# Kernel optimization log

Hardware: AMD Instinct MI355X
Metric: run time of the kernel (lower is better)

Reference implementation:

```python
import jax, jax.numpy as jnp
import numpy as np
import math

B, H, L, DK, D, LOCAL = 4, 8, 2048, 64, 512, 4


def setup_inputs() -> dict:
    key = jax.random.key(0)
    ks = jax.random.split(key, 9)
    n = L
    return {
        'query': jax.random.normal(ks[0], (B, H, L, DK), jnp.float32),
        'key': jax.random.normal(ks[1], (B, H, L, DK), jnp.float32),
        'value': jax.random.normal(ks[2], (B, H, L, DK), jnp.float32),
        'users': jax.random.normal(ks[3], (B, L, D), jnp.float32),
        'mask': jnp.tril(jnp.ones((L, L), dtype=bool))[None, None],  # causal [1,1,L,L]
        'rel_pos_w': jax.random.normal(ks[4], (2 * n - 1, DK * LOCAL), jnp.float32) * 0.02,
        'user_proj_w': jax.random.normal(ks[5], (DK * LOCAL, D), jnp.float32) * 0.02,
        'user_proj_b': jax.random.normal(ks[6], (DK * LOCAL,), jnp.float32) * 0.02,
        'mlp_w': jax.random.normal(ks[7], (LOCAL, DK), jnp.float32) * 0.1,
        'mlp_b': jax.random.normal(ks[8], (LOCAL,), jnp.float32) * 0.1,
    }


def reference(query, key, value, users, mask, rel_pos_w, user_proj_w, user_proj_b, mlp_w, mlp_b):
    b, h, l, dk = query.shape
    local = mlp_w.shape[0]
    g = h - local
    n = l
    scale = 1.0 / math.sqrt(dk)
    NEG = -1e12  # MAX_VAL in the torch source

    # ---- global heads: plain softmax attention ----
    qg, kg, vg = query[:, :g], key[:, :g], value[:, :g]
    sg = jnp.einsum('bhqd,bhkd->bhqk', qg, kg) * scale
    sg = jnp.where(mask, sg, NEG)
    pg = jax.nn.softmax(sg, axis=-1)
    og = jnp.einsum('bhqk,bhkd->bhqd', pg, vg)

    # ---- local (LOCKER) heads ----
    ql, kl, vl = query[:, g:], key[:, g:], value[:, g:]
    sl = jnp.einsum('bhqd,bhkd->bhqk', ql, kl) * scale

    # reweight = Linear(d_k,1)(rel_pos + v_q + v_k + user_proj(users)_q) per local head.
    # Linear over a sum decomposes exactly (same math, avoids [b,local,l,l,dk] tensor):
    rel_tab = rel_pos_w.reshape(2 * n - 1, local, dk)
    rel_scores = jnp.einsum('rhd,hd->rh', rel_tab, mlp_w)          # [2n-1, local]
    pos = jnp.arange(n)
    distance = pos[None, :] - pos[:, None] + n - 1                  # [l, l]
    rel_term = rel_scores[distance].transpose(2, 0, 1)              # [local, l, l]

    v_term = jnp.einsum('bhkd,hd->bhk', vl, mlp_w)                  # [b, local, l]
    u = (users @ user_proj_w.T + user_proj_b).reshape(b, l, local, dk)
    u_term = jnp.einsum('bqhd,hd->bhq', u, mlp_w)                   # [b, local, l]

    reweight = (rel_term[None]
                + v_term[:, :, None, :]      # value_l.unsqueeze(-3): varies over key idx
                + v_term[:, :, :, None]      # value_l.unsqueeze(-2): varies over query idx
                + u_term[:, :, :, None]      # user term broadcast over key idx
                + mlp_b[None, :, None, None])

    sl = sl + reweight
    sl = jnp.where(mask, sl, NEG)
    pl = jax.nn.softmax(sl, axis=-1)
    ol = jnp.einsum('bhqk,bhkd->bhqd', pl, vl)

    return jnp.concatenate([og, ol], axis=1)  # [b, h, l, d_k]
```

## Files before the change

### kernel.cpp

```cpp
#include <hip/hip_runtime.h>

#define TL 2048
#define NHEAD 8
#define NLOC 4
#define L2E 1.44269504f
#define PSTRIDE 4352

typedef __attribute__((ext_vector_type(4))) float f32x4;
typedef __attribute__((ext_vector_type(16))) float f32x16;
typedef __attribute__((ext_vector_type(8))) __bf16 bf16x8;
typedef __attribute__((ext_vector_type(8))) unsigned short u16x8;
typedef __attribute__((ext_vector_type(4))) unsigned int u32x4;

static __device__ __forceinline__ unsigned short f2bf(float f) {
    unsigned u = __float_as_uint(f);
    u = (u + 0x7FFFu + ((u >> 16) & 1u)) >> 16;
    return (unsigned short)u;
}
static __device__ __forceinline__ unsigned int cvtpk(float a, float b) {
    unsigned int w;
    asm("v_cvt_pk_bf16_f32 %0, %1, %2" : "=v"(w) : "v"(a), "v"(b));
    return w;
}

__global__ __launch_bounds__(256) void preconv_kernel(
    const float* __restrict__ key, const float* __restrict__ value,
    const float* __restrict__ mlp_w, const float* __restrict__ rel_pos_w,
    unsigned short* __restrict__ Kb, unsigned short* __restrict__ Vtb,
    float* __restrict__ vtbf, float* __restrict__ rel_sf) {
    int blk = blockIdx.x;
    int t = threadIdx.x;
    int wave = t >> 6, lane = t & 63;

    if (blk >= 1024) {
        int r = (blk - 1024) * 4 + wave;
        if (r < 2 * TL - 1) {
#pragma unroll
            for (int hp = 0; hp < 4; ++hp) {
                float v = rel_pos_w[r * 256 + hp * 64 + lane] * mlp_w[hp * 64 + lane];
#pragma unroll
                for (int off = 32; off; off >>= 1) v += __shfl_xor(v, off);
                if (lane == 0) rel_sf[hp * 4096 + r] = v * L2E;
            }
        }
        return;
    }

    __shared__ float Tf[64][66];
    int bh = blk >> 5, kt = blk & 31;
    int h = bh & 7, b = bh >> 3;
    size_t src = (size_t)blk * 4096;
    size_t dst = (size_t)blk * 4096;

    {
        int row = t >> 2, q4 = t & 3;
        const float* kp = key + src + row * 64 + q4 * 16;
#pragma unroll
        for (int j = 0; j < 4; ++j)
            *(f32x4*)&Tf[row][q4 * 16 + j * 4] = *(const f32x4*)(kp + j * 4);
    }
    __syncthreads();
#pragma unroll
    for (int i = 0; i < 2; ++i) {
        int idx = t + i * 256;
        int l31 = idx & 31, hi = (idx >> 5) & 1, mq = (idx >> 6) & 3, h2 = idx >> 8;
        int r = h2 * 32 + l31, c = mq * 2 + hi;
        u16x8 o;
#pragma unroll
        for (int j = 0; j < 8; ++j) o[j] = f2bf(Tf[r][c * 8 + j]);
        *(u16x8*)&Kb[dst + idx * 8] = o;
    }
    __syncthreads();

    {
        int row = t >> 2, q4 = t & 3;
        const float* vp = value + src + row * 64 + q4 * 16;
#pragma unroll
        for (int j = 0; j < 4; ++j)
            *(f32x4*)&Tf[row][q4 * 16 + j * 4] = *(const f32x4*)(vp + j * 4);
    }
    __syncthreads();
#pragma unroll
    for (int i = 0; i < 2; ++i) {
        int idx = t + i * 256;
        int l31 = idx & 31, hi = (idx >> 5) & 1, half = (idx >> 6) & 1, c2 = idx >> 7;
        int r = half * 32 + l31, c = c2 * 2 + hi;
        u16x8 o;
#pragma unroll
        for (int j = 0; j < 8; ++j) o[j] = f2bf(Tf[c * 8 + j][r]);
        *(u16x8*)&Vtb[dst + idx * 8] = o;
    }
    if (h >= NLOC) {
        float mw = mlp_w[(h - NLOC) * 64 + lane];
        float* vout = vtbf + (size_t)((b * NLOC + h - NLOC) * TL) + kt * 64;
#pragma unroll
        for (int i = 0; i < 16; ++i) {
            int row = wave * 16 + i;
            float v = Tf[row][lane] * mw;
#pragma unroll
            for (int off = 32; off; off >>= 1) v += __shfl_xor(v, off);
            if (lane == 0) vout[row] = v * L2E;
        }
    }
}

#define MFMA32(A, B, C) __builtin_amdgcn_mfma_f32_32x32x16_bf16(A, B, C, 0, 0, 0)

__global__ __launch_bounds__(256, 4) void attn_kernel(
    const float* __restrict__ query,
    const unsigned short* __restrict__ Kb, const unsigned short* __restrict__ Vtb,
    const float* __restrict__ rel_sf, const float* __restrict__ vtbf,
    float* __restrict__ part) {

    __shared__ float relw[384];

    int bid = blockIdx.x;
    int bhx = bid & 31;
    int bh = (bhx & 7) * 4 + (bhx >> 3);
    int sid = bid >> 5;
    int i = 0, s = 0, acc = 0;
    for (int ii = 15; ii >= 0; --ii) {
        int ns = (2 * ii + 4) / 3;
        if (sid >= acc && sid < acc + ns) { i = ii; s = sid - acc; }
        acc += ns;
    }
    int nt = 2 * i + 2;
    int n = (2 * i + 4) / 3;
    int T = nt / n, R = nt % n;
    int k_b = s * T + min(s, R);
    int len = T + (s < R ? 1 : 0);
    int q0 = i << 7;

    int h = bh & 7, b = bh >> 3;
    bool islocal = (h >= NLOC);
    int t = threadIdx.x;
    int w = t >> 6;
    int l31 = t & 31;
    int hi = (t >> 5) & 1;
    int qrel = 32 * w + l31;
    int qglob = q0 + qrel;
    int qmaxw = q0 + 32 * w + 31;
    int hivl = hi * 256 + l31 * 8;

    size_t tbase = (size_t)bh * 32 * 4096;
    const unsigned short* Ktiles = Kb + tbase;
    const unsigned short* Vtiles = Vtb + tbase;
    const float* vtpf = vtbf + (islocal ? (size_t)((b * NLOC + h - NLOC) * TL) : 0);
    int idxlo = 64 * k_b - q0 + 1920;
    const float* relsrc = rel_sf + (islocal ? ((h - NLOC) * 4096 + idxlo) : 0);

    if (islocal && t < 96) ((f32x4*)relw)[t] = ((const f32x4*)relsrc)[t];

    const float SC = 0.125f * L2E;
    bf16x8 qf[4];
    {
        const float* qsrc = query + ((size_t)bh * TL + qglob) * 64 + 8 * hi;
#pragma unroll
        for (int mq = 0; mq < 4; ++mq) {
            f32x4 a = *(const f32x4*)(qsrc + 16 * mq);
            f32x4 c = *(const f32x4*)(qsrc + 16 * mq + 4);
            u16x8 u;
#pragma unroll
            for (int j = 0; j < 4; ++j) { u[j] = f2bf(a[j] * SC); u[4 + j] = f2bf(c[j] * SC); }
            qf[mq] = __builtin_bit_cast(bf16x8, u);
        }
    }

    float m = -1e30f, lsum = 0.f;
    f32x16 O0 = {0,0,0,0,0,0,0,0,0,0,0,0,0,0,0,0};
    f32x16 O1 = {0,0,0,0,0,0,0,0,0,0,0,0,0,0,0,0};

    __syncthreads();

#pragma unroll 1
    for (int kt4 = 0; kt4 < len; ++kt4) {
        int kt = k_b + kt4;
        if (64 * kt > qmaxw) break;
        const unsigned short* Kt = Ktiles + (size_t)kt * 4096;
        const unsigned short* Vt = Vtiles + (size_t)kt * 4096;
        const float* bias = vtpf + kt * 64;
        bool maskt = (64 * kt + 63 > q0 + 32 * w);

#pragma unroll
        for (int h2 = 0; h2 < 2; ++h2) {
            f32x16 S;
            if (islocal) {
                int rbase = 64 * kt4 + 32 * h2 + 4 * hi + 127 - qrel;
#pragma unroll
                for (int g = 0; g < 4; ++g) {
                    f32x4 bv = *(const f32x4*)&bias[32 * h2 + 8 * g + 4 * hi];
#pragma unroll
                    for (int j = 0; j < 4; ++j)
                        S[4 * g + j] = bv[j] + relw[rbase + 8 * g + j];
                }
            } else {
                S = (f32x16){0,0,0,0,0,0,0,0,0,0,0,0,0,0,0,0};
            }
            __builtin_amdgcn_s_setprio(1);
#pragma unroll
            for (int mq = 0; mq < 4; ++mq) {
                const bf16x8 kf = *(const bf16x8*)&Kt[(h2 * 4 + mq) * 512 + hivl];
                S = MFMA32(kf, qf[mq], S);
            }
            __builtin_amdgcn_s_setprio(0);

            if (maskt) {
                int koff = 64 * kt + 32 * h2 + 4 * hi - qglob;
#pragma unroll
                for (int r = 0; r < 16; ++r) {
                    int kk = (r & 3) + 8 * (r >> 2);
                    if (koff + kk > 0) S[r] = -1e30f;
                }
            }
            float pmax = -1e30f;
#pragma unroll
            for (int r = 0; r < 16; ++r) pmax = fmaxf(pmax, S[r]);
            pmax = fmaxf(pmax, __shfl_xor(pmax, 32));
            if (__any(pmax > m + 11.5f)) {
                float nm2 = fmaxf(m, pmax);
                float corr = exp2f(m - nm2);
                lsum *= corr;
#pragma unroll
                for (int r = 0; r < 16; ++r) { O0[r] *= corr; O1[r] *= corr; }
                m = nm2;
            }
            float ps = 0.f;
#pragma unroll
            for (int r = 0; r < 16; ++r) {
                float p = exp2f(S[r] - m);
                S[r] = p; ps += p;
            }
            ps += __shfl_xor(ps, 32);
            lsum += ps;

            __builtin_amdgcn_s_setprio(1);
#pragma unroll
            for (int kq = 0; kq < 2; ++kq) {
                int ra = 8 * kq;
                unsigned int x0 = cvtpk(S[ra + 0], S[ra + 1]);
                unsigned int x1 = cvtpk(S[ra + 2], S[ra + 3]);
                unsigned int y0 = cvtpk(S[ra + 4], S[ra + 5]);
                unsigned int y1 = cvtpk(S[ra + 6], S[ra + 7]);
                asm("v_permlane32_swap_b32 %0, %1" : "+v"(x0), "+v"(y0));
                asm("v_permlane32_swap_b32 %0, %1" : "+v"(x1), "+v"(y1));
                u32x4 fw;
                fw[0] = x0; fw[1] = x1; fw[2] = y0; fw[3] = y1;
                const bf16x8 pf = __builtin_bit_cast(bf16x8, fw);
                int c2 = h2 * 2 + kq;
                const bf16x8 vf0 = *(const bf16x8*)&Vt[c2 * 1024 + hivl];
                const bf16x8 vf1 = *(const bf16x8*)&Vt[c2 * 1024 + 512 + hivl];
                O0 = MFMA32(vf0, pf, O0);
                O1 = MFMA32(vf1, pf, O1);
            }
            __builtin_amdgcn_s_setprio(0);
        }
    }

    float* pp = part + (size_t)bid * PSTRIDE;
    unsigned int* po = (unsigned int*)pp;
#pragma unroll
    for (int g = 0; g < 4; ++g) {
        unsigned int w0 = cvtpk(O0[4 * g + 0], O0[4 * g + 1]);
        unsigned int w1 = cvtpk(O0[4 * g + 2], O0[4 * g + 3]);
        unsigned int w2 = cvtpk(O1[4 * g + 0], O1[4 * g + 1]);
        unsigned int w3 = cvtpk(O1[4 * g + 2], O1[4 * g + 3]);
        int dp0 = 4 * g + 2 * hi;
        po[dp0 * 128 + qrel] = w0;
        po[(dp0 + 1) * 128 + qrel] = w1;
        po[(16 + dp0) * 128 + qrel] = w2;
        po[(16 + dp0 + 1) * 128 + qrel] = w3;
    }
    if (hi == 0) { pp[4096 + qrel] = m; pp[4224 + qrel] = lsum; }
}

__global__ __launch_bounds__(128) void merge_kernel(
    const float* __restrict__ part, float* __restrict__ out) {
    int bid = blockIdx.x;
    int bhx = bid & 31, i = bid >> 5;
    int bh = (bhx & 7) * 4 + (bhx >> 3);
    int n = (2 * i + 4) / 3;
    int sb = 0;
    for (int ii = 15; ii > i; --ii) sb += (2 * ii + 4) / 3;
    int t = threadIdx.x;

    float mv[11], lv[11];
#pragma unroll
    for (int s2 = 0; s2 < 11; ++s2) {
        mv[s2] = -1e30f; lv[s2] = 0.f;
        if (s2 < n) {
            const float* pp = part + (size_t)((sb + s2) * 32 + bhx) * PSTRIDE;
            mv[s2] = pp[4096 + t]; lv[s2] = pp[4224 + t];
        }
    }
    float nm = mv[0];
#pragma unroll
    for (int s2 = 1; s2 < 11; ++s2) nm = fmaxf(nm, mv[s2]);
    float den = 0.f;
    float cw[11];
#pragma unroll
    for (int s2 = 0; s2 < 11; ++s2) { cw[s2] = exp2f(mv[s2] - nm); den += lv[s2] * cw[s2]; }
    float inv = 1.0f / den;
#pragma unroll
    for (int s2 = 0; s2 < 11; ++s2) cw[s2] *= inv;

    size_t obase = (size_t)bh * TL * 64 + (size_t)(128 * i + t) * 64;
    for (int seg = 0; seg < 4; ++seg) {
        float o[16];
#pragma unroll
        for (int j = 0; j < 16; ++j) o[j] = 0.f;
#pragma unroll
        for (int s2 = 0; s2 < 11; ++s2) {
            if (s2 < n) {
                const unsigned int* po =
                    (const unsigned int*)(part + (size_t)((sb + s2) * 32 + bhx) * PSTRIDE);
                float wsc = cw[s2];
#pragma unroll
                for (int j = 0; j < 8; ++j) {
                    unsigned int wv = po[(seg * 8 + j) * 128 + t];
                    o[2 * j]     += wsc * __uint_as_float((wv & 0xffffu) << 16);
                    o[2 * j + 1] += wsc * __uint_as_float(wv & 0xffff0000u);
                }
            }
        }
#pragma unroll
        for (int c = 0; c < 4; ++c)
            *(f32x4*)(out + obase + seg * 16 + 4 * c) = *(const f32x4*)&o[4 * c];
    }
}

extern "C" void kernel_launch(void* const* d_in, const int* in_sizes, int n_in,
                              void* d_out, int out_size, void* d_ws, size_t ws_size,
                              hipStream_t stream) {
    const float* query = (const float*)d_in[0];
    const float* key = (const float*)d_in[1];
    const float* value = (const float*)d_in[2];
    const float* rel_pos_w = (const float*)d_in[5];
    const float* mlp_w = (const float*)d_in[8];
    float* out = (float*)d_out;

    unsigned short* Kb = (unsigned short*)d_ws;
    unsigned short* Vtb = Kb + 32 * 32 * 4096;
    float* rel_sf = (float*)(Vtb + 32 * 32 * 4096);
    float* vtbf = rel_sf + 4 * 4096;
    float* part = vtbf + 32768;

    preconv_kernel<<<2048, 256, 0, stream>>>(key, value, mlp_w, rel_pos_w,
                                             Kb, Vtb, vtbf, rel_sf);
    attn_kernel<<<3072, 256, 0, stream>>>(query, Kb, Vtb, rel_sf, vtbf, part);
    merge_kernel<<<512, 128, 0, stream>>>(part, out);
}
```

Measured before the change: 90.48 us.

## Double-buffer K/V tiles in LDS via async global loads and halve KV splits

Attention blocks now stage each K and V tile into LDS with global_load_lds in a double buffer, prefetching the next tile while the current one is computed, and synchronising once per tile. The number of KV splits per query block roughly halves, giving a smaller grid where each block handles more tiles and the merge kernel combines fewer partials. This targets global-load latency and split/merge overhead, at the cost of about 34KB of LDS per block (lower occupancy), a barrier per tile, and less parallelism.

```diff
diff --git a/kernel.cpp b/kernel.cpp
--- a/kernel.cpp
+++ b/kernel.cpp
@@ -21,6 +21,11 @@
     unsigned int w;
     asm("v_cvt_pk_bf16_f32 %0, %1, %2" : "=v"(w) : "v"(a), "v"(b));
     return w;
+}
+static __device__ __forceinline__ void gl_lds16(const void* g, void* l) {
+    __builtin_amdgcn_global_load_lds(
+        (const __attribute__((address_space(1))) void*)g,
+        (__attribute__((address_space(3))) void*)l, 16, 0, 0);
 }
 
 __global__ __launch_bounds__(256) void preconv_kernel(
@@ -112,7 +117,10 @@
     const float* __restrict__ rel_sf, const float* __restrict__ vtbf,
     float* __restrict__ part) {
 
-    __shared__ float relw[384];
+    __shared__ __align__(16) unsigned char smem[34816];
+    unsigned short* Ks0 = (unsigned short*)smem;
+    unsigned short* Vt0 = (unsigned short*)(smem + 16384);
+    float* relw = (float*)(smem + 32768);
 
     int bid = blockIdx.x;
     int bhx = bid & 31;
@@ -120,12 +128,12 @@
     int sid = bid >> 5;
     int i = 0, s = 0, acc = 0;
     for (int ii = 15; ii >= 0; --ii) {
-        int ns = (2 * ii + 4) / 3;
+        int ns = (2 * ii + 7) / 6;
         if (sid >= acc && sid < acc + ns) { i = ii; s = sid - acc; }
         acc += ns;
     }
     int nt = 2 * i + 2;
-    int n = (2 * i + 4) / 3;
+    int n = (2 * i + 7) / 6;
     int T = nt / n, R = nt % n;
     int k_b = s * T + min(s, R);
     int len = T + (s < R ? 1 : 0);
@@ -149,7 +157,11 @@
     int idxlo = 64 * k_b - q0 + 1920;
     const float* relsrc = rel_sf + (islocal ? ((h - NLOC) * 4096 + idxlo) : 0);
 
-    if (islocal && t < 96) ((f32x4*)relw)[t] = ((const f32x4*)relsrc)[t];
+    gl_lds16(Ktiles + (size_t)k_b * 4096 + t * 8, Ks0 + t * 8);
+    gl_lds16(Ktiles + (size_t)k_b * 4096 + 2048 + t * 8, Ks0 + 2048 + t * 8);
+    gl_lds16(Vtiles + (size_t)k_b * 4096 + t * 8, Vt0 + t * 8);
+    gl_lds16(Vtiles + (size_t)k_b * 4096 + 2048 + t * 8, Vt0 + 2048 + t * 8);
+    if (islocal && t < 128) ((f32x4*)relw)[t] = ((const f32x4*)relsrc)[t];
 
     const float SC = 0.125f * L2E;
     bf16x8 qf[4];
@@ -172,88 +184,103 @@
 
     __syncthreads();
 
+    int cur = 0;
 #pragma unroll 1
     for (int kt4 = 0; kt4 < len; ++kt4) {
         int kt = k_b + kt4;
-        if (64 * kt > qmaxw) break;
-        const unsigned short* Kt = Ktiles + (size_t)kt * 4096;
-        const unsigned short* Vt = Vtiles + (size_t)kt * 4096;
+        unsigned short* Ks = Ks0 + cur * 4096;
+        unsigned short* Vt = Vt0 + cur * 4096;
         const float* bias = vtpf + kt * 64;
+
+        if (kt4 + 1 < len) {
+            int nb = cur ^ 1;
+            const unsigned short* gk = Ktiles + (size_t)(kt + 1) * 4096;
+            const unsigned short* gv = Vtiles + (size_t)(kt + 1) * 4096;
+            gl_lds16(gk + t * 8, Ks0 + nb * 4096 + t * 8);
+            gl_lds16(gk + 2048 + t * 8, Ks0 + nb * 4096 + 2048 + t * 8);
+            gl_lds16(gv + t * 8, Vt0 + nb * 4096 + t * 8);
+            gl_lds16(gv + 2048 + t * 8, Vt0 + nb * 4096 + 2048 + t * 8);
+        }
+
+        bool active = (64 * kt <= qmaxw);
         bool maskt = (64 * kt + 63 > q0 + 32 * w);
-
-#pragma unroll
-        for (int h2 = 0; h2 < 2; ++h2) {
-            f32x16 S;
-            if (islocal) {
-                int rbase = 64 * kt4 + 32 * h2 + 4 * hi + 127 - qrel;
-#pragma unroll
-                for (int g = 0; g < 4; ++g) {
-                    f32x4 bv = *(const f32x4*)&bias[32 * h2 + 8 * g + 4 * hi];
-#pragma unroll
-                    for (int j = 0; j < 4; ++j)
-                        S[4 * g + j] = bv[j] + relw[rbase + 8 * g + j];
-                }
-            } else {
-                S = (f32x16){0,0,0,0,0,0,0,0,0,0,0,0,0,0,0,0};
+        if (active) {
+#pragma unroll
+            for (int h2 = 0; h2 < 2; ++h2) {
+                f32x16 S;
+                if (islocal) {
+                    int rbase = 64 * kt4 + 32 * h2 + 4 * hi + 127 - qrel;
+#pragma unroll
+                    for (int g = 0; g < 4; ++g) {
+                        f32x4 bv = *(const f32x4*)&bias[32 * h2 + 8 * g + 4 * hi];
+#pragma unroll
+                        for (int j = 0; j < 4; ++j)
+                            S[4 * g + j] = bv[j] + relw[rbase + 8 * g + j];
+                    }
+                } else {
+                    S = (f32x16){0,0,0,0,0,0,0,0,0,0,0,0,0,0,0,0};
+                }
+                __builtin_amdgcn_s_setprio(1);
+#pragma unroll
+                for (int mq = 0; mq < 4; ++mq) {
+                    const bf16x8 kf = *(const bf16x8*)&Ks[(h2 * 4 + mq) * 512 + hivl];
+                    S = MFMA32(kf, qf[mq], S);
+                }
+                __builtin_amdgcn_s_setprio(0);
+
+                if (maskt) {
+                    int koff = 64 * kt + 32 * h2 + 4 * hi - qglob;
+#pragma unroll
+                    for (int r = 0; r < 16; ++r) {
+                        int kk = (r & 3) + 8 * (r >> 2);
+                        if (koff + kk > 0) S[r] = -1e30f;
+                    }
+                }
+                float pmax = -1e30f;
+#pragma unroll
+                for (int r = 0; r < 16; ++r) pmax = fmaxf(pmax, S[r]);
+                pmax = fmaxf(pmax, __shfl_xor(pmax, 32));
+                if (__any(pmax > m + 11.5f)) {
+                    float nm2 = fmaxf(m, pmax);
+                    float corr = exp2f(m - nm2);
+                    lsum *= corr;
+#pragma unroll
+                    for (int r = 0; r < 16; ++r) { O0[r] *= corr; O1[r] *= corr; }
+                    m = nm2;
+                }
+                float ps = 0.f;
+#pragma unroll
+                for (int r = 0; r < 16; ++r) {
+                    float p = exp2f(S[r] - m);
+                    S[r] = p; ps += p;
+                }
+                ps += __shfl_xor(ps, 32);
+                lsum += ps;
+
+                __builtin_amdgcn_s_setprio(1);
+#pragma unroll
+                for (int kq = 0; kq < 2; ++kq) {
+                    int ra = 8 * kq;
+                    unsigned int x0 = cvtpk(S[ra + 0], S[ra + 1]);
+                    unsigned int x1 = cvtpk(S[ra + 2], S[ra + 3]);
+                    unsigned int y0 = cvtpk(S[ra + 4], S[ra + 5]);
+                    unsigned int y1 = cvtpk(S[ra + 6], S[ra + 7]);
+                    asm("v_permlane32_swap_b32 %0, %1" : "+v"(x0), "+v"(y0));
+                    asm("v_permlane32_swap_b32 %0, %1" : "+v"(x1), "+v"(y1));
+                    u32x4 fw;
+                    fw[0] = x0; fw[1] = x1; fw[2] = y0; fw[3] = y1;
+                    const bf16x8 pf = __builtin_bit_cast(bf16x8, fw);
+                    int c2 = h2 * 2 + kq;
+                    const bf16x8 vf0 = *(const bf16x8*)&Vt[c2 * 1024 + hivl];
+                    const bf16x8 vf1 = *(const bf16x8*)&Vt[c2 * 1024 + 512 + hivl];
+                    O0 = MFMA32(vf0, pf, O0);
+                    O1 = MFMA32(vf1, pf, O1);
+                }
+                __builtin_amdgcn_s_setprio(0);
             }
-            __builtin_amdgcn_s_setprio(1);
-#pragma unroll
-            for (int mq = 0; mq < 4; ++mq) {
-                const bf16x8 kf = *(const bf16x8*)&Kt[(h2 * 4 + mq) * 512 + hivl];
-                S = MFMA32(kf, qf[mq], S);
-            }
-            __builtin_amdgcn_s_setprio(0);
-
-            if (maskt) {
-                int koff = 64 * kt + 32 * h2 + 4 * hi - qglob;
-#pragma unroll
-                for (int r = 0; r < 16; ++r) {
-                    int kk = (r & 3) + 8 * (r >> 2);
-                    if (koff + kk > 0) S[r] = -1e30f;
-                }
-            }
-            float pmax = -1e30f;
-#pragma unroll
-            for (int r = 0; r < 16; ++r) pmax = fmaxf(pmax, S[r]);
-            pmax = fmaxf(pmax, __shfl_xor(pmax, 32));
-            if (__any(pmax > m + 11.5f)) {
-                float nm2 = fmaxf(m, pmax);
-                float corr = exp2f(m - nm2);
-                lsum *= corr;
-#pragma unroll
-                for (int r = 0; r < 16; ++r) { O0[r] *= corr; O1[r] *= corr; }
-                m = nm2;
-            }
-            float ps = 0.f;
-#pragma unroll
-            for (int r = 0; r < 16; ++r) {
-                float p = exp2f(S[r] - m);
-                S[r] = p; ps += p;
-            }
-            ps += __shfl_xor(ps, 32);
-            lsum += ps;
-
-            __builtin_amdgcn_s_setprio(1);
-#pragma unroll
-            for (int kq = 0; kq < 2; ++kq) {
-                int ra = 8 * kq;
-                unsigned int x0 = cvtpk(S[ra + 0], S[ra + 1]);
-                unsigned int x1 = cvtpk(S[ra + 2], S[ra + 3]);
-                unsigned int y0 = cvtpk(S[ra + 4], S[ra + 5]);
-                unsigned int y1 = cvtpk(S[ra + 6], S[ra + 7]);
-                asm("v_permlane32_swap_b32 %0, %1" : "+v"(x0), "+v"(y0));
-                asm("v_permlane32_swap_b32 %0, %1" : "+v"(x1), "+v"(y1));
-                u32x4 fw;
-                fw[0] = x0; fw[1] = x1; fw[2] = y0; fw[3] = y1;
-                const bf16x8 pf = __builtin_bit_cast(bf16x8, fw);
-                int c2 = h2 * 2 + kq;
-                const bf16x8 vf0 = *(const bf16x8*)&Vt[c2 * 1024 + hivl];
-                const bf16x8 vf1 = *(const bf16x8*)&Vt[c2 * 1024 + 512 + hivl];
-                O0 = MFMA32(vf0, pf, O0);
-                O1 = MFMA32(vf1, pf, O1);
-            }
-            __builtin_amdgcn_s_setprio(0);
-        }
+        }
+        __syncthreads();
+        cur ^= 1;
     }
 
     float* pp = part + (size_t)bid * PSTRIDE;
@@ -278,14 +305,14 @@
     int bid = blockIdx.x;
     int bhx = bid & 31, i = bid >> 5;
     int bh = (bhx & 7) * 4 + (bhx >> 3);
-    int n = (2 * i + 4) / 3;
+    int n = (2 * i + 7) / 6;
     int sb = 0;
-    for (int ii = 15; ii > i; --ii) sb += (2 * ii + 4) / 3;
+    for (int ii = 15; ii > i; --ii) sb += (2 * ii + 7) / 6;
     int t = threadIdx.x;
 
-    float mv[11], lv[11];
-#pragma unroll
-    for (int s2 = 0; s2 < 11; ++s2) {
+    float mv[6], lv[6];
+#pragma unroll
+    for (int s2 = 0; s2 < 6; ++s2) {
         mv[s2] = -1e30f; lv[s2] = 0.f;
         if (s2 < n) {
             const float* pp = part + (size_t)((sb + s2) * 32 + bhx) * PSTRIDE;
@@ -294,14 +321,14 @@
     }
     float nm = mv[0];
 #pragma unroll
-    for (int s2 = 1; s2 < 11; ++s2) nm = fmaxf(nm, mv[s2]);
+    for (int s2 = 1; s2 < 6; ++s2) nm = fmaxf(nm, mv[s2]);
     float den = 0.f;
-    float cw[11];
-#pragma unroll
-    for (int s2 = 0; s2 < 11; ++s2) { cw[s2] = exp2f(mv[s2] - nm); den += lv[s2] * cw[s2]; }
+    float cw[6];
+#pragma unroll
+    for (int s2 = 0; s2 < 6; ++s2) { cw[s2] = exp2f(mv[s2] - nm); den += lv[s2] * cw[s2]; }
     float inv = 1.0f / den;
 #pragma unroll
-    for (int s2 = 0; s2 < 11; ++s2) cw[s2] *= inv;
+    for (int s2 = 0; s2 < 6; ++s2) cw[s2] *= inv;
 
     size_t obase = (size_t)bh * TL * 64 + (size_t)(128 * i + t) * 64;
     for (int seg = 0; seg < 4; ++seg) {
@@ -309,7 +336,7 @@
 #pragma unroll
         for (int j = 0; j < 16; ++j) o[j] = 0.f;
 #pragma unroll
-        for (int s2 = 0; s2 < 11; ++s2) {
+        for (int s2 = 0; s2 < 6; ++s2) {
             if (s2 < n) {
                 const unsigned int* po =
                     (const unsigned int*)(part + (size_t)((sb + s2) * 32 + bhx) * PSTRIDE);
@@ -346,6 +373,6 @@
 
     preconv_kernel<<<2048, 256, 0, stream>>>(key, value, mlp_w, rel_pos_w,
                                              Kb, Vtb, vtbf, rel_sf);
-    attn_kernel<<<3072, 256, 0, stream>>>(query, Kb, Vtb, rel_sf, vtbf, part);
+    attn_kernel<<<1632, 256, 0, stream>>>(query, Kb, Vtb, rel_sf, vtbf, part);
     merge_kernel<<<512, 128, 0, stream>>>(part, out);
 }
```

Measured after the change: 77.85 us. -14.0%, faster.
